# Kernel tuning notes

Measured on AMD Instinct MI355X. Metric: run time of the kernel, lower is better.

The kernel has to match this reference:

```python
import jax, jax.numpy as jnp
import numpy as np

B, N, D, H, DH = 4, 2048, 512, 8, 64  # batch, seqlen, hidden, heads, dim-per-head
EPS = 1e-5


def _layer_norm(x, g, b):
    m = jnp.mean(x, axis=-1, keepdims=True)
    v = jnp.var(x, axis=-1, keepdims=True)
    return (x - m) * jax.lax.rsqrt(v + EPS) * g + b


def setup_inputs() -> dict:
    key = jax.random.key(0)
    k0, k1, k2 = jax.random.split(key, 3)
    T = B * N
    return {
        "x": jax.random.normal(k0, (T, D), jnp.float32),
        "ln1_g": jnp.ones((D,), jnp.float32),
        "ln1_b": jnp.zeros((D,), jnp.float32),
        "w_uvqk": jax.random.normal(k1, (D, H * 4 * DH), jnp.float32) * 0.02,
        "ln2_g": jnp.ones((H * DH,), jnp.float32),
        "ln2_b": jnp.zeros((H * DH,), jnp.float32),
        "w_proj": jax.random.normal(k2, (H * DH, D), jnp.float32) * 0.02,
        "scaling_seqlen": N,
    }


def reference(x, ln1_g, ln1_b, w_uvqk, ln2_g, ln2_b, w_proj, scaling_seqlen):
    T = x.shape[0]
    # input layernorm -> fused uvqk projection -> SiLU
    normed_x = _layer_norm(x, ln1_g, ln1_b)
    silu_uvqk = jax.nn.silu(normed_x @ w_uvqk)          # [T, H*4*DH]
    silu_uvqk = silu_uvqk.reshape(T, H, 4 * DH)
    user, value, query, key = jnp.split(silu_uvqk, [DH, 2 * DH, 3 * DH], axis=-1)

    # jagged -> [B, N, H, DH] (equal-length sequences, offsets = i*N)
    q = query.reshape(B, N, H, DH)
    k = key.reshape(B, N, H, DH)
    v = value.reshape(B, N, H, DH)

    # HSTU attention: silu-gated (no softmax), causal, scaled by 1/scaling_seqlen
    scores = jnp.einsum('bnhd,bmhd->bhnm', q, k)        # [B, H, N, N]
    p = jax.nn.silu(scores) / jnp.float32(scaling_seqlen)
    causal = jnp.tril(jnp.ones((N, N), bool))
    p = jnp.where(causal, p, 0.0)
    attn = jnp.einsum('bhnm,bmhd->bnhd', p, v).reshape(T, H * DH)

    # output norm, user gate, projection, residual (dropout p=0.0 -> identity)
    normed_attn = _layer_norm(attn, ln2_g, ln2_b)
    user_flat = user.reshape(T, H * DH)
    out = (normed_attn * user_flat) @ w_proj + x
    return out
```

## Files before the change

kernel.cpp:

```cpp
#include <hip/hip_runtime.h>
#include <hip/hip_bf16.h>

typedef __bf16 bf16;
typedef __attribute__((ext_vector_type(8))) __bf16 bf16x8;
typedef __attribute__((ext_vector_type(4))) float f32x4;
typedef __attribute__((ext_vector_type(16))) float f32x16;

#define BB   4
#define NN   2048
#define DD   512
#define HH   8
#define DHH  64
#define TT   (BB*NN)
#define NUU  (HH*4*DHH)

#define AS1 __attribute__((address_space(1)))
#define AS3 __attribute__((address_space(3)))
__device__ __forceinline__ void gload16(const void* g, void* l){
  __builtin_amdgcn_global_load_lds((const AS1 void*)g, (AS3 void*)l, 16, 0, 0);
}

__device__ __forceinline__ float silu_fast(float x){
  return x * __builtin_amdgcn_rcpf(1.0f + __expf(-x));
}

__device__ __forceinline__ unsigned pk2(float a, float b){
  return (unsigned)__builtin_bit_cast(unsigned short, (bf16)a)
       | ((unsigned)__builtin_bit_cast(unsigned short, (bf16)b) << 16);
}

__device__ __forceinline__ void plswap(unsigned &a, unsigned &b){
  asm volatile("v_permlane32_swap_b32 %0, %1" : "+v"(a), "+v"(b));
}

__constant__ unsigned ATBL[24] = {
  7u|(0u<<4)|(16u<<10), 15u|(0u<<4)|(16u<<10), 14u|(0u<<4)|(15u<<10), 14u|(15u<<4)|(15u<<10),
  6u|(0u<<4)|(14u<<10), 13u|(0u<<4)|(14u<<10), 12u|(0u<<4)|(13u<<10), 11u|(0u<<4)|(12u<<10),
  15u|(16u<<4)|(16u<<10), 13u|(14u<<4)|(14u<<10), 12u|(13u<<4)|(13u<<10), 10u|(0u<<4)|(11u<<10),
  10u|(11u<<4)|(11u<<10), 9u|(0u<<4)|(10u<<10), 5u|(0u<<4)|(12u<<10), 11u|(12u<<4)|(12u<<10),
  0u|(0u<<4)|(2u<<10), 1u|(0u<<4)|(4u<<10), 2u|(0u<<4)|(6u<<10), 3u|(0u<<4)|(8u<<10),
  8u|(0u<<4)|(9u<<10), 9u|(10u<<4)|(10u<<10), 8u|(9u<<4)|(9u<<10), 4u|(0u<<4)|(10u<<10)
};

__global__ void k_pre(const float* __restrict__ w1, bf16* __restrict__ o1,
                      const float* __restrict__ w2, bf16* __restrict__ o2,
                      const float* __restrict__ x, const float* __restrict__ g,
                      const float* __restrict__ bta, bf16* __restrict__ xn){
  int bx = blockIdx.x;
  int t  = threadIdx.x;
  if (bx < 1280){
    __shared__ float tile[32][33];
    int tx = t & 31, ty = t >> 5;
    int bx2 = bx % 80, by = bx / 80;
    const float* in; bf16* out; int R, C, c0;
    if (bx2 < 64){ in = w1; out = o1; R = 512; C = 2048; c0 = bx2*32; }
    else         { in = w2; out = o2; R = 512; C = 512;  c0 = (bx2-64)*32; }
    int r0 = by*32;
    #pragma unroll
    for (int i=0;i<4;i++) tile[ty+i*8][tx] = in[(size_t)(r0+ty+i*8)*C + c0+tx];
    __syncthreads();
    #pragma unroll
    for (int i=0;i<4;i++) out[(size_t)(c0+ty+i*8)*R + r0+tx] = (bf16)tile[tx][ty+i*8];
  } else {
    int lane = t & 63;
    int row  = (bx-1280)*4 + (t>>6);
    const float* xr = x + (size_t)row*512 + lane*8;
    float4 v0 = *(const float4*)xr;
    float4 v1 = *(const float4*)(xr+4);
    float vv[8] = {v0.x,v0.y,v0.z,v0.w,v1.x,v1.y,v1.z,v1.w};
    float s = 0.f, ss = 0.f;
    #pragma unroll
    for (int j=0;j<8;j++){ s += vv[j]; ss += vv[j]*vv[j]; }
    #pragma unroll
    for (int d=32; d; d>>=1){ s += __shfl_xor(s,d); ss += __shfl_xor(ss,d); }
    float m  = s * (1.f/512.f);
    float vr = ss * (1.f/512.f) - m*m;
    float rs = rsqrtf(vr + 1e-5f);
    const float* gp = g + lane*8;
    const float* bp = bta + lane*8;
    bf16x8 o;
    #pragma unroll
    for (int j=0;j<8;j++) o[j] = (bf16)((vv[j]-m)*rs*gp[j] + bp[j]);
    *(bf16x8*)(xn + (size_t)row*512 + lane*8) = o;
  }
}

__global__ void k_ln_gate(const float* __restrict__ attn0, const float* __restrict__ attn1,
                          const float* __restrict__ g, const float* __restrict__ bta,
                          const bf16* __restrict__ uvqk, bf16* __restrict__ out){
  int lane = threadIdx.x & 63;
  int row  = blockIdx.x*4 + (threadIdx.x>>6);
  const float* xr = attn0 + (size_t)row*512 + lane*8;
  float4 v0 = *(const float4*)xr;
  float4 v1 = *(const float4*)(xr+4);
  float vv[8] = {v0.x,v0.y,v0.z,v0.w,v1.x,v1.y,v1.z,v1.w};
  if (((row & (NN-1)) >> 7) >= 8){
    const float* x2 = attn1 + (size_t)row*512 + lane*8;
    float4 w0 = *(const float4*)x2;
    float4 w1 = *(const float4*)(x2+4);
    vv[0]+=w0.x; vv[1]+=w0.y; vv[2]+=w0.z; vv[3]+=w0.w;
    vv[4]+=w1.x; vv[5]+=w1.y; vv[6]+=w1.z; vv[7]+=w1.w;
  }
  float s = 0.f, ss = 0.f;
  #pragma unroll
  for (int j=0;j<8;j++){ s += vv[j]; ss += vv[j]*vv[j]; }
  #pragma unroll
  for (int d=32; d; d>>=1){ s += __shfl_xor(s,d); ss += __shfl_xor(ss,d); }
  float m  = s * (1.f/512.f);
  float vr = ss * (1.f/512.f) - m*m;
  float rs = rsqrtf(vr + 1e-5f);
  const float* gp = g + lane*8;
  const float* bp = bta + lane*8;
  const bf16* up = uvqk + (size_t)row*NUU + (lane>>3)*256 + ((lane*8)&63);
  bf16x8 uu = *(const bf16x8*)up;
  bf16x8 o;
  #pragma unroll
  for (int j=0;j<8;j++)
    o[j] = (bf16)(((vv[j]-m)*rs*gp[j] + bp[j]) * (float)uu[j]);
  *(bf16x8*)(out + (size_t)row*512 + lane*8) = o;
}

template<int EPI>
__global__ __launch_bounds__(256) void k_gemm(const bf16* __restrict__ A,
                                              const bf16* __restrict__ BT,
                                              int Nd, const float* __restrict__ resid,
                                              void* __restrict__ Cout,
                                              bf16* __restrict__ vtout){
  __shared__ __align__(16) char smem[32768];
  char* As = smem;
  char* Bs = smem + 16384;
  const int K = 512;
  int t = threadIdx.x, lane = t & 63, wid = t >> 6;
  int wr = wid >> 1, wc = wid & 1;
  int lin = blockIdx.x;
  int wk  = (lin & 7)*((int)gridDim.x >> 3) + (lin >> 3);
  int nx  = Nd >> 7;
  int m0 = (wk / nx) * 128, n0 = (wk % nx) * 128;
  int blk = (lane & 7) ^ (lane >> 3);
  const bf16* gA = A  + (size_t)(m0 + wid*32 + (lane>>3))*K + blk*8;
  const bf16* gB = BT + (size_t)(n0 + wid*32 + (lane>>3))*K + blk*8;
  f32x4 acc[4][4] = {};
  for (int k0 = 0; k0 < K; k0 += 64){
    __syncthreads();
    #pragma unroll
    for (int c = 0; c < 4; ++c){
      gload16(gA + (size_t)c*8*K, As + wid*4096 + c*1024);
      gload16(gB + (size_t)c*8*K, Bs + wid*4096 + c*1024);
    }
    gA += 64; gB += 64;
    __syncthreads();
    #pragma unroll
    for (int kk = 0; kk < 64; kk += 32){
      int c0 = kk + (lane >> 4) * 8;
      bf16x8 a[4], b[4];
      #pragma unroll
      for (int i = 0; i < 4; i++){
        int ra = wr*64 + i*16 + (lane & 15);
        a[i] = *(const bf16x8*)(As + (((ra*64 + c0)*2) ^ ((ra & 7) << 4)));
        int rb = wc*64 + i*16 + (lane & 15);
        b[i] = *(const bf16x8*)(Bs + (((rb*64 + c0)*2) ^ ((rb & 7) << 4)));
      }
      #pragma unroll
      for (int i = 0; i < 4; i++)
        #pragma unroll
        for (int jj = 0; jj < 4; jj++)
          acc[i][jj] = __builtin_amdgcn_mfma_f32_16x16x32_bf16(a[i], b[jj], acc[i][jj], 0, 0, 0);
    }
  }
  bool isv = (EPI == 0) && ((n0 & 255) == 0) && (wc == 1);
  #pragma unroll
  for (int i = 0; i < 4; i++){
    #pragma unroll
    for (int jj = 0; jj < 4; jj++){
      int col = n0 + wc*64 + jj*16 + (lane & 15);
      if (EPI == 0){
        union { unsigned long long u; ushort s[4]; } pw;
        #pragma unroll
        for (int r = 0; r < 4; r++){
          int rowg = m0 + wr*64 + i*16 + (lane >> 4)*4 + r;
          float sv = silu_fast(acc[i][jj][r]);
          ((bf16*)Cout)[(size_t)rowg*Nd + col] = (bf16)sv;
          pw.s[r] = __builtin_bit_cast(ushort, (bf16)sv);
        }
        if (isv){
          int dh    = jj*16 + (lane & 15);
          int rowg0 = m0 + wr*64 + i*16 + (lane >> 4)*4;
          int bb = rowg0 >> 11, nn = rowg0 & (NN-1);
          int hh = n0 >> 8;
          *(unsigned long long*)(vtout + ((size_t)((bb*HH + hh)*64 + dh)*NN + nn)) = pw.u;
        }
      } else {
        #pragma unroll
        for (int r = 0; r < 4; r++){
          int rowg = m0 + wr*64 + i*16 + (lane >> 4)*4 + r;
          ((float*)Cout)[(size_t)rowg*Nd + col] = acc[i][jj][r] + resid[(size_t)rowg*Nd + col];
        }
      }
    }
  }
}

__global__ __launch_bounds__(256, 4) void k_attn(const bf16* __restrict__ uv,
                                                 const bf16* __restrict__ vt,
                                                 float* __restrict__ attn0,
                                                 float* __restrict__ attn1,
                                                 const int* __restrict__ scal){
  __shared__ __align__(16) char smem[32768];
  int t = threadIdx.x, lane = t & 63, w = t >> 6;
  int hi5 = lane >> 5;
  int l31 = lane & 31;
  int lin = blockIdx.x;
  int pos = lin & 255;
  int grp = pos & 31;
  int rank = (lin >> 8)*8 + (pos >> 5);
  unsigned e = ATBL[rank];
  int qt = e & 15;
  int j0 = (int)((e >> 4) & 63);
  int j1 = j0 + (int)(e >> 10) - 1;
  float* ob = j0 ? attn1 : attn0;
  int b = grp >> 3, h = grp & 7;
  int tok0 = b*NN + qt*128;
  float sinv = 1.0f / (float)(scal[0]);

  int blk  = (lane & 7) ^ (lane >> 3);
  int rsub = lane >> 3;

  bf16x8 qfrag[4];
  {
    const bf16* gq = uv + (size_t)(tok0 + w*32 + l31)*NUU + h*256 + 128 + hi5*8;
    #pragma unroll
    for (int ks = 0; ks < 4; ++ks)
      qfrag[ks] = *(const bf16x8*)(gq + ks*16);
  }
  const bf16* gk = uv + (size_t)(b*NN + j0*64 + w*16 + rsub)*NUU + h*256 + 192 + blk*8;
  const bf16* gv = vt + (size_t)((b*HH + h)*64 + w*16 + rsub)*NN + j0*64 + blk*8;
  gload16(gk,                  smem + w*2048);
  gload16(gk + (size_t)8*NUU,  smem + w*2048 + 1024);
  gload16(gv,                  smem + 8192 + w*2048);
  gload16(gv + (size_t)8*NN,   smem + 8192 + w*2048 + 1024);
  gk += (size_t)64*NUU; gv += 64;

  f32x16 oacc[2] = {};
  int qmin  = qt*128 + w*32;
  int qglob = qmin + l31;
  int cur = 0;
  for (int j = j0; j <= j1; ++j){
    if (j < j1){
      gload16(gk,                 smem + (cur^1)*16384 + w*2048);
      gload16(gk + (size_t)8*NUU, smem + (cur^1)*16384 + w*2048 + 1024);
      gload16(gv,                 smem + (cur^1)*16384 + 8192 + w*2048);
      gload16(gv + (size_t)8*NN,  smem + (cur^1)*16384 + 8192 + w*2048 + 1024);
      gk += (size_t)64*NUU; gv += 64;
      asm volatile("s_waitcnt vmcnt(4)" ::: "memory");
    } else {
      asm volatile("s_waitcnt vmcnt(0)" ::: "memory");
    }
    __builtin_amdgcn_s_barrier();
    const char* Ks = smem + cur*16384;
    const char* Vs = Ks + 8192;
    #pragma unroll
    for (int sub = 0; sub < 2; ++sub){
      int kvbase = j*64 + sub*32;
      if (kvbase < qmin + 32){
        f32x16 sacc = {};
        int rk = sub*32 + l31;
        #pragma unroll
        for (int ks = 0; ks < 4; ++ks){
          int c0 = ks*16 + hi5*8;
          bf16x8 ak = *(const bf16x8*)(Ks + (((rk*64 + c0)*2) ^ ((rk & 7) << 4)));
          sacc = __builtin_amdgcn_mfma_f32_32x32x16_bf16(ak, qfrag[ks], sacc, 0, 0, 0);
        }
        union { unsigned u[8]; bf16x8 v[2]; } P;
        if (kvbase + 31 <= qmin){
          #pragma unroll
          for (int m = 0; m < 4; ++m){
            P.u[2*m]   = pk2(silu_fast(sacc[4*m+0]), silu_fast(sacc[4*m+1]));
            P.u[2*m+1] = pk2(silu_fast(sacc[4*m+2]), silu_fast(sacc[4*m+3]));
          }
        } else {
          #pragma unroll
          for (int m = 0; m < 4; ++m){
            float pr[4];
            #pragma unroll
            for (int r = 0; r < 4; ++r){
              int kvg = kvbase + 8*m + 4*hi5 + r;
              pr[r] = (kvg <= qglob) ? silu_fast(sacc[4*m+r]) : 0.0f;
            }
            P.u[2*m]   = pk2(pr[0], pr[1]);
            P.u[2*m+1] = pk2(pr[2], pr[3]);
          }
        }
        plswap(P.u[0], P.u[2]); plswap(P.u[1], P.u[3]);
        plswap(P.u[4], P.u[6]); plswap(P.u[5], P.u[7]);
        #pragma unroll
        for (int kh = 0; kh < 2; ++kh){
          int c0 = sub*32 + kh*16 + hi5*8;
          #pragma unroll
          for (int dsb = 0; dsb < 2; ++dsb){
            int rv = dsb*32 + l31;
            bf16x8 vb = *(const bf16x8*)(Vs + (((rv*64 + c0)*2) ^ ((rv & 7) << 4)));
            oacc[dsb] = __builtin_amdgcn_mfma_f32_32x32x16_bf16(P.v[kh], vb, oacc[dsb], 0, 0, 0);
          }
        }
      }
    }
    asm volatile("" ::: "memory");
    __builtin_amdgcn_s_barrier();
    cur ^= 1;
  }
  #pragma unroll
  for (int dsb = 0; dsb < 2; ++dsb){
    #pragma unroll
    for (int r = 0; r < 16; ++r){
      int qrow = (r & 3) + 4*hi5 + 8*(r >> 2);
      ob[(size_t)(tok0 + w*32 + qrow)*DD + h*64 + dsb*32 + l31] = oacc[dsb][r] * sinv;
    }
  }
}

extern "C" void kernel_launch(void* const* d_in, const int* in_sizes, int n_in,
                              void* d_out, int out_size, void* d_ws, size_t ws_size,
                              hipStream_t stream){
  (void)in_sizes; (void)n_in; (void)out_size; (void)ws_size;
  const float* x      = (const float*)d_in[0];
  const float* ln1_g  = (const float*)d_in[1];
  const float* ln1_b  = (const float*)d_in[2];
  const float* w_uvqk = (const float*)d_in[3];
  const float* ln2_g  = (const float*)d_in[4];
  const float* ln2_b  = (const float*)d_in[5];
  const float* w_proj = (const float*)d_in[6];
  const int*   scal   = (const int*)d_in[7];
  float* out = (float*)d_out;

  char* ws = (char*)d_ws;
  bf16*  wT1  = (bf16*)(ws);
  bf16*  wT2  = (bf16*)(ws + (2u<<20));
  bf16*  xn   = (bf16*)(ws + (2u<<20) + (512u<<10));
  bf16*  uvq  = (bf16*)(ws + (10u<<20) + (512u<<10));
  float* attn0= (float*)(ws + (42u<<20) + (512u<<10));
  bf16*  vtb  = (bf16*)(ws + (58u<<20) + (512u<<10));
  float* attn1= (float*)(ws + (66u<<20) + (512u<<10));

  k_pre<<<dim3(3328), dim3(256), 0, stream>>>(w_uvqk, wT1, w_proj, wT2,
                                              x, ln1_g, ln1_b, xn);
  k_gemm<0><<<dim3(1024), dim3(256), 0, stream>>>(xn, wT1, 2048, nullptr, (void*)uvq, vtb);
  k_attn<<<dim3(768), dim3(256), 0, stream>>>(uvq, vtb, attn0, attn1, scal);
  k_ln_gate<<<TT/4, 256, 0, stream>>>(attn0, attn1, ln2_g, ln2_b, uvq, xn);
  k_gemm<1><<<dim3(256), dim3(256), 0, stream>>>(xn, wT2, 512, x, (void*)out, nullptr);
}
```

Baseline: 95.36 us.

## Rebalance causal attention work with multi-item schedule and four partial buffers

Replaces the one-item-per-block work table with a table of up to three work items per block. Query tiles are split into up to four KV-range chunks, each written to its own partial-sum buffer. The goal is to even out per-block causal work across the 768 blocks and cut tail imbalance. In exchange it adds extra partial outputs that the LN-gate kernel must read and sum, which means more memory traffic, plus a per-item reload of Q and a pipeline restart.

```diff
diff --git a/kernel.cpp b/kernel.cpp
--- a/kernel.cpp
+++ b/kernel.cpp
@@ -33,13 +33,32 @@
   asm volatile("v_permlane32_swap_b32 %0, %1" : "+v"(a), "+v"(b));
 }
 
-__constant__ unsigned ATBL[24] = {
-  7u|(0u<<4)|(16u<<10), 15u|(0u<<4)|(16u<<10), 14u|(0u<<4)|(15u<<10), 14u|(15u<<4)|(15u<<10),
-  6u|(0u<<4)|(14u<<10), 13u|(0u<<4)|(14u<<10), 12u|(0u<<4)|(13u<<10), 11u|(0u<<4)|(12u<<10),
-  15u|(16u<<4)|(16u<<10), 13u|(14u<<4)|(14u<<10), 12u|(13u<<4)|(13u<<10), 10u|(0u<<4)|(11u<<10),
-  10u|(11u<<4)|(11u<<10), 9u|(0u<<4)|(10u<<10), 5u|(0u<<4)|(12u<<10), 11u|(12u<<4)|(12u<<10),
-  0u|(0u<<4)|(2u<<10), 1u|(0u<<4)|(4u<<10), 2u|(0u<<4)|(6u<<10), 3u|(0u<<4)|(8u<<10),
-  8u|(0u<<4)|(9u<<10), 9u|(10u<<4)|(10u<<10), 8u|(9u<<4)|(9u<<10), 4u|(0u<<4)|(10u<<10)
+#define ITEM(q,j,c,bu) ((unsigned)((q)|((j)<<4)|((c)<<10)|((bu)<<16)))
+__constant__ unsigned WTBL[72] = {
+  ITEM(0,0,2,0),   ITEM(1,0,4,0),  ITEM(2,0,6,0),
+  ITEM(3,0,8,0),   ITEM(4,0,4,0),  0,
+  ITEM(4,4,6,1),   ITEM(5,0,6,0),  0,
+  ITEM(5,6,6,1),   ITEM(6,0,6,0),  0,
+  ITEM(6,6,8,1),   ITEM(7,0,4,0),  0,
+  ITEM(7,4,12,1),  0,              0,
+  ITEM(8,0,12,0),  0,              0,
+  ITEM(8,12,6,1),  ITEM(9,0,6,0),  0,
+  ITEM(9,6,12,1),  0,              0,
+  ITEM(9,18,2,2),  ITEM(10,0,10,0),0,
+  ITEM(10,10,12,1),0,              0,
+  ITEM(11,0,12,0), 0,              0,
+  ITEM(11,12,12,1),0,              0,
+  ITEM(12,12,12,1),0,              0,
+  ITEM(13,10,12,1),0,              0,
+  ITEM(13,22,6,2), ITEM(14,0,6,0), 0,
+  ITEM(15,0,8,0),  0,              0,
+  ITEM(15,8,8,1),  0,              0,
+  ITEM(15,16,8,2), 0,              0,
+  ITEM(15,24,8,3), 0,              0,
+  ITEM(12,0,12,0), 0,              0,
+  ITEM(12,24,2,2), ITEM(13,0,10,0),0,
+  ITEM(14,6,12,1), 0,              0,
+  ITEM(14,18,12,2),0,              0
 };
 
 __global__ void k_pre(const float* __restrict__ w1, bf16* __restrict__ o1,
@@ -85,19 +104,30 @@
   }
 }
 
-__global__ void k_ln_gate(const float* __restrict__ attn0, const float* __restrict__ attn1,
+__global__ void k_ln_gate(const float* __restrict__ a0, const float* __restrict__ a1,
+                          const float* __restrict__ a2, const float* __restrict__ a3,
                           const float* __restrict__ g, const float* __restrict__ bta,
                           const bf16* __restrict__ uvqk, bf16* __restrict__ out){
   int lane = threadIdx.x & 63;
   int row  = blockIdx.x*4 + (threadIdx.x>>6);
-  const float* xr = attn0 + (size_t)row*512 + lane*8;
-  float4 v0 = *(const float4*)xr;
-  float4 v1 = *(const float4*)(xr+4);
+  size_t off = (size_t)row*512 + lane*8;
+  float4 v0 = *(const float4*)(a0 + off);
+  float4 v1 = *(const float4*)(a0 + off + 4);
   float vv[8] = {v0.x,v0.y,v0.z,v0.w,v1.x,v1.y,v1.z,v1.w};
-  if (((row & (NN-1)) >> 7) >= 8){
-    const float* x2 = attn1 + (size_t)row*512 + lane*8;
-    float4 w0 = *(const float4*)x2;
-    float4 w1 = *(const float4*)(x2+4);
+  int qtile = (row & (NN-1)) >> 7;
+  int np = (int)((0x4333223222221111ULL >> (qtile*4)) & 15);
+  if (np >= 2){
+    float4 w0 = *(const float4*)(a1 + off), w1 = *(const float4*)(a1 + off + 4);
+    vv[0]+=w0.x; vv[1]+=w0.y; vv[2]+=w0.z; vv[3]+=w0.w;
+    vv[4]+=w1.x; vv[5]+=w1.y; vv[6]+=w1.z; vv[7]+=w1.w;
+  }
+  if (np >= 3){
+    float4 w0 = *(const float4*)(a2 + off), w1 = *(const float4*)(a2 + off + 4);
+    vv[0]+=w0.x; vv[1]+=w0.y; vv[2]+=w0.z; vv[3]+=w0.w;
+    vv[4]+=w1.x; vv[5]+=w1.y; vv[6]+=w1.z; vv[7]+=w1.w;
+  }
+  if (np >= 4){
+    float4 w0 = *(const float4*)(a3 + off), w1 = *(const float4*)(a3 + off + 4);
     vv[0]+=w0.x; vv[1]+=w0.y; vv[2]+=w0.z; vv[3]+=w0.w;
     vv[4]+=w1.x; vv[5]+=w1.y; vv[6]+=w1.z; vv[7]+=w1.w;
   }
@@ -117,7 +147,7 @@
   #pragma unroll
   for (int j=0;j<8;j++)
     o[j] = (bf16)(((vv[j]-m)*rs*gp[j] + bp[j]) * (float)uu[j]);
-  *(bf16x8*)(out + (size_t)row*512 + lane*8) = o;
+  *(bf16x8*)(out + off) = o;
 }
 
 template<int EPI>
@@ -202,8 +232,10 @@
 
 __global__ __launch_bounds__(256, 4) void k_attn(const bf16* __restrict__ uv,
                                                  const bf16* __restrict__ vt,
-                                                 float* __restrict__ attn0,
-                                                 float* __restrict__ attn1,
+                                                 float* __restrict__ a0,
+                                                 float* __restrict__ a1,
+                                                 float* __restrict__ a2,
+                                                 float* __restrict__ a3,
                                                  const int* __restrict__ scal){
   __shared__ __align__(16) char smem[32768];
   int t = threadIdx.x, lane = t & 63, w = t >> 6;
@@ -213,107 +245,112 @@
   int pos = lin & 255;
   int grp = pos & 31;
   int rank = (lin >> 8)*8 + (pos >> 5);
-  unsigned e = ATBL[rank];
-  int qt = e & 15;
-  int j0 = (int)((e >> 4) & 63);
-  int j1 = j0 + (int)(e >> 10) - 1;
-  float* ob = j0 ? attn1 : attn0;
   int b = grp >> 3, h = grp & 7;
-  int tok0 = b*NN + qt*128;
   float sinv = 1.0f / (float)(scal[0]);
 
   int blk  = (lane & 7) ^ (lane >> 3);
   int rsub = lane >> 3;
-
-  bf16x8 qfrag[4];
-  {
-    const bf16* gq = uv + (size_t)(tok0 + w*32 + l31)*NUU + h*256 + 128 + hi5*8;
-    #pragma unroll
-    for (int ks = 0; ks < 4; ++ks)
-      qfrag[ks] = *(const bf16x8*)(gq + ks*16);
-  }
-  const bf16* gk = uv + (size_t)(b*NN + j0*64 + w*16 + rsub)*NUU + h*256 + 192 + blk*8;
-  const bf16* gv = vt + (size_t)((b*HH + h)*64 + w*16 + rsub)*NN + j0*64 + blk*8;
-  gload16(gk,                  smem + w*2048);
-  gload16(gk + (size_t)8*NUU,  smem + w*2048 + 1024);
-  gload16(gv,                  smem + 8192 + w*2048);
-  gload16(gv + (size_t)8*NN,   smem + 8192 + w*2048 + 1024);
-  gk += (size_t)64*NUU; gv += 64;
-
-  f32x16 oacc[2] = {};
-  int qmin  = qt*128 + w*32;
-  int qglob = qmin + l31;
   int cur = 0;
-  for (int j = j0; j <= j1; ++j){
-    if (j < j1){
-      gload16(gk,                 smem + (cur^1)*16384 + w*2048);
-      gload16(gk + (size_t)8*NUU, smem + (cur^1)*16384 + w*2048 + 1024);
-      gload16(gv,                 smem + (cur^1)*16384 + 8192 + w*2048);
-      gload16(gv + (size_t)8*NN,  smem + (cur^1)*16384 + 8192 + w*2048 + 1024);
-      gk += (size_t)64*NUU; gv += 64;
-      asm volatile("s_waitcnt vmcnt(4)" ::: "memory");
-    } else {
-      asm volatile("s_waitcnt vmcnt(0)" ::: "memory");
-    }
-    __builtin_amdgcn_s_barrier();
-    const char* Ks = smem + cur*16384;
-    const char* Vs = Ks + 8192;
-    #pragma unroll
-    for (int sub = 0; sub < 2; ++sub){
-      int kvbase = j*64 + sub*32;
-      if (kvbase < qmin + 32){
-        f32x16 sacc = {};
-        int rk = sub*32 + l31;
-        #pragma unroll
-        for (int ks = 0; ks < 4; ++ks){
-          int c0 = ks*16 + hi5*8;
-          bf16x8 ak = *(const bf16x8*)(Ks + (((rk*64 + c0)*2) ^ ((rk & 7) << 4)));
-          sacc = __builtin_amdgcn_mfma_f32_32x32x16_bf16(ak, qfrag[ks], sacc, 0, 0, 0);
-        }
-        union { unsigned u[8]; bf16x8 v[2]; } P;
-        if (kvbase + 31 <= qmin){
+
+  for (int it = 0; it < 3; ++it){
+    unsigned e = WTBL[rank*3 + it];
+    if (!e) break;
+    int qt   = (int)(e & 15);
+    int j0   = (int)((e >> 4) & 63);
+    int j1   = j0 + (int)((e >> 10) & 63) - 1;
+    int bsel = (int)((e >> 16) & 3);
+    int tok0 = b*NN + qt*128;
+
+    bf16x8 qfrag[4];
+    {
+      const bf16* gq = uv + (size_t)(tok0 + w*32 + l31)*NUU + h*256 + 128 + hi5*8;
+      #pragma unroll
+      for (int ks = 0; ks < 4; ++ks)
+        qfrag[ks] = *(const bf16x8*)(gq + ks*16);
+    }
+    const bf16* gk = uv + (size_t)(b*NN + j0*64 + w*16 + rsub)*NUU + h*256 + 192 + blk*8;
+    const bf16* gv = vt + (size_t)((b*HH + h)*64 + w*16 + rsub)*NN + j0*64 + blk*8;
+    gload16(gk,                  smem + cur*16384 + w*2048);
+    gload16(gk + (size_t)8*NUU,  smem + cur*16384 + w*2048 + 1024);
+    gload16(gv,                  smem + cur*16384 + 8192 + w*2048);
+    gload16(gv + (size_t)8*NN,   smem + cur*16384 + 8192 + w*2048 + 1024);
+    gk += (size_t)64*NUU; gv += 64;
+
+    f32x16 oacc[2] = {};
+    int qmin  = qt*128 + w*32;
+    int qglob = qmin + l31;
+    for (int j = j0; j <= j1; ++j){
+      if (j < j1){
+        gload16(gk,                 smem + (cur^1)*16384 + w*2048);
+        gload16(gk + (size_t)8*NUU, smem + (cur^1)*16384 + w*2048 + 1024);
+        gload16(gv,                 smem + (cur^1)*16384 + 8192 + w*2048);
+        gload16(gv + (size_t)8*NN,  smem + (cur^1)*16384 + 8192 + w*2048 + 1024);
+        gk += (size_t)64*NUU; gv += 64;
+        asm volatile("s_waitcnt vmcnt(4)" ::: "memory");
+      } else {
+        asm volatile("s_waitcnt vmcnt(0)" ::: "memory");
+      }
+      __builtin_amdgcn_s_barrier();
+      const char* Ks = smem + cur*16384;
+      const char* Vs = Ks + 8192;
+      #pragma unroll
+      for (int sub = 0; sub < 2; ++sub){
+        int kvbase = j*64 + sub*32;
+        if (kvbase < qmin + 32){
+          f32x16 sacc = {};
+          int rk = sub*32 + l31;
           #pragma unroll
-          for (int m = 0; m < 4; ++m){
-            P.u[2*m]   = pk2(silu_fast(sacc[4*m+0]), silu_fast(sacc[4*m+1]));
-            P.u[2*m+1] = pk2(silu_fast(sacc[4*m+2]), silu_fast(sacc[4*m+3]));
+          for (int ks = 0; ks < 4; ++ks){
+            int c0 = ks*16 + hi5*8;
+            bf16x8 ak = *(const bf16x8*)(Ks + (((rk*64 + c0)*2) ^ ((rk & 7) << 4)));
+            sacc = __builtin_amdgcn_mfma_f32_32x32x16_bf16(ak, qfrag[ks], sacc, 0, 0, 0);
           }
-        } else {
+          union { unsigned u[8]; bf16x8 v[2]; } P;
+          if (kvbase + 31 <= qmin){
+            #pragma unroll
+            for (int m = 0; m < 4; ++m){
+              P.u[2*m]   = pk2(silu_fast(sacc[4*m+0]), silu_fast(sacc[4*m+1]));
+              P.u[2*m+1] = pk2(silu_fast(sacc[4*m+2]), silu_fast(sacc[4*m+3]));
+            }
+          } else {
+            #pragma unroll
+            for (int m = 0; m < 4; ++m){
+              float pr[4];
+              #pragma unroll
+              for (int r = 0; r < 4; ++r){
+                int kvg = kvbase + 8*m + 4*hi5 + r;
+                pr[r] = (kvg <= qglob) ? silu_fast(sacc[4*m+r]) : 0.0f;
+              }
+              P.u[2*m]   = pk2(pr[0], pr[1]);
+              P.u[2*m+1] = pk2(pr[2], pr[3]);
+            }
+          }
+          plswap(P.u[0], P.u[2]); plswap(P.u[1], P.u[3]);
+          plswap(P.u[4], P.u[6]); plswap(P.u[5], P.u[7]);
           #pragma unroll
-          for (int m = 0; m < 4; ++m){
-            float pr[4];
+          for (int kh = 0; kh < 2; ++kh){
+            int c0 = sub*32 + kh*16 + hi5*8;
             #pragma unroll
-            for (int r = 0; r < 4; ++r){
-              int kvg = kvbase + 8*m + 4*hi5 + r;
-              pr[r] = (kvg <= qglob) ? silu_fast(sacc[4*m+r]) : 0.0f;
+            for (int dsb = 0; dsb < 2; ++dsb){
+              int rv = dsb*32 + l31;
+              bf16x8 vb = *(const bf16x8*)(Vs + (((rv*64 + c0)*2) ^ ((rv & 7) << 4)));
+              oacc[dsb] = __builtin_amdgcn_mfma_f32_32x32x16_bf16(P.v[kh], vb, oacc[dsb], 0, 0, 0);
             }
-            P.u[2*m]   = pk2(pr[0], pr[1]);
-            P.u[2*m+1] = pk2(pr[2], pr[3]);
           }
         }
-        plswap(P.u[0], P.u[2]); plswap(P.u[1], P.u[3]);
-        plswap(P.u[4], P.u[6]); plswap(P.u[5], P.u[7]);
-        #pragma unroll
-        for (int kh = 0; kh < 2; ++kh){
-          int c0 = sub*32 + kh*16 + hi5*8;
-          #pragma unroll
-          for (int dsb = 0; dsb < 2; ++dsb){
-            int rv = dsb*32 + l31;
-            bf16x8 vb = *(const bf16x8*)(Vs + (((rv*64 + c0)*2) ^ ((rv & 7) << 4)));
-            oacc[dsb] = __builtin_amdgcn_mfma_f32_32x32x16_bf16(P.v[kh], vb, oacc[dsb], 0, 0, 0);
-          }
-        }
-      }
-    }
-    asm volatile("" ::: "memory");
-    __builtin_amdgcn_s_barrier();
-    cur ^= 1;
-  }
-  #pragma unroll
-  for (int dsb = 0; dsb < 2; ++dsb){
-    #pragma unroll
-    for (int r = 0; r < 16; ++r){
-      int qrow = (r & 3) + 4*hi5 + 8*(r >> 2);
-      ob[(size_t)(tok0 + w*32 + qrow)*DD + h*64 + dsb*32 + l31] = oacc[dsb][r] * sinv;
+      }
+      asm volatile("" ::: "memory");
+      __builtin_amdgcn_s_barrier();
+      cur ^= 1;
+    }
+    float* ob = (bsel==0) ? a0 : (bsel==1) ? a1 : (bsel==2) ? a2 : a3;
+    #pragma unroll
+    for (int dsb = 0; dsb < 2; ++dsb){
+      #pragma unroll
+      for (int r = 0; r < 16; ++r){
+        int qrow = (r & 3) + 4*hi5 + 8*(r >> 2);
+        ob[(size_t)(tok0 + w*32 + qrow)*DD + h*64 + dsb*32 + l31] = oacc[dsb][r] * sinv;
+      }
     }
   }
 }
@@ -340,11 +377,13 @@
   float* attn0= (float*)(ws + (42u<<20) + (512u<<10));
   bf16*  vtb  = (bf16*)(ws + (58u<<20) + (512u<<10));
   float* attn1= (float*)(ws + (66u<<20) + (512u<<10));
+  float* attn2= (float*)(ws + (82u<<20) + (512u<<10));
+  float* attn3= (float*)(ws + (98u<<20) + (512u<<10));
 
   k_pre<<<dim3(3328), dim3(256), 0, stream>>>(w_uvqk, wT1, w_proj, wT2,
                                               x, ln1_g, ln1_b, xn);
   k_gemm<0><<<dim3(1024), dim3(256), 0, stream>>>(xn, wT1, 2048, nullptr, (void*)uvq, vtb);
-  k_attn<<<dim3(768), dim3(256), 0, stream>>>(uvq, vtb, attn0, attn1, scal);
-  k_ln_gate<<<TT/4, 256, 0, stream>>>(attn0, attn1, ln2_g, ln2_b, uvq, xn);
+  k_attn<<<dim3(768), dim3(256), 0, stream>>>(uvq, vtb, attn0, attn1, attn2, attn3, scal);
+  k_ln_gate<<<TT/4, 256, 0, stream>>>(attn0, attn1, attn2, attn3, ln2_g, ln2_b, uvq, xn);
   k_gemm<1><<<dim3(256), dim3(256), 0, stream>>>(xn, wT2, 512, x, (void*)out, nullptr);
 }
```

Result: slower. 97.95 us (+2.7%).
